# Kernel tuning notes

Hardware: AMD Instinct MI355X
Metric: run time of the kernel (lower is better)

## Reference

```python
import jax, jax.numpy as jnp
import numpy as np

GROUPS = 32
EPS = 1e-5
N_HEADS = 4


def group_norm(x, w, b):
    # x: [B, C, T]; GroupNorm over (C/G, T) within each of G groups
    B, C, T = x.shape
    xg = x.reshape(B, GROUPS, (C // GROUPS) * T)
    mean = xg.mean(axis=-1, keepdims=True)
    var = xg.var(axis=-1, keepdims=True)
    xn = ((xg - mean) * jax.lax.rsqrt(var + EPS)).reshape(B, C, T)
    return xn * w[None, :, None] + b[None, :, None]


def setup_inputs() -> dict:
    key = jax.random.key(0)
    ks = jax.random.split(key, 5)
    B, C, H, W = 2, 256, 64, 64
    x = jax.random.normal(ks[0], (B, C, H, W), dtype=jnp.float32)
    norm_w = jnp.ones((C,), dtype=jnp.float32)
    norm_b = jnp.zeros((C,), dtype=jnp.float32)
    qkv_w = jax.random.normal(ks[1], (3 * C, C), dtype=jnp.float32) * (C ** -0.5)
    qkv_b = jax.random.normal(ks[2], (3 * C,), dtype=jnp.float32) * 0.02
    proj_w = jax.random.normal(ks[3], (C, C), dtype=jnp.float32) * (C ** -0.5)
    proj_b = jax.random.normal(ks[4], (C,), dtype=jnp.float32) * 0.02
    return {"x": x, "norm_w": norm_w, "norm_b": norm_b,
            "qkv_w": qkv_w, "qkv_b": qkv_b,
            "proj_w": proj_w, "proj_b": proj_b}


def reference(x, norm_w, norm_b, qkv_w, qkv_b, proj_w, proj_b):
    B, C, Hs, Ws = x.shape
    T = Hs * Ws
    xf = x.reshape(B, C, T)
    xn = group_norm(xf, norm_w, norm_b)
    # 1x1 conv1d == channel matmul: [3C,C] x [B,C,T] -> [B,3C,T]
    qkv = jnp.einsum('oc,bct->bot', qkv_w, xn) + qkv_b[None, :, None]
    ch = C // N_HEADS
    # legacy order: [B, H*3*ch, T] -> [B*H, 3*ch, T] -> split
    qkv_h = qkv.reshape(B * N_HEADS, 3 * ch, T)
    q, k, v = qkv_h[:, :ch], qkv_h[:, ch:2 * ch], qkv_h[:, 2 * ch:]
    scale = ch ** -0.25
    # full [B*H, T, T] score matrix, softmax in fp32 (faithful to source)
    weight = jnp.einsum('bct,bcs->bts', q * scale, k * scale)
    weight = jax.nn.softmax(weight.astype(jnp.float32), axis=-1).astype(qkv.dtype)
    a = jnp.einsum('bts,bcs->bct', weight, v).reshape(B, C, T)
    h = jnp.einsum('oc,bct->bot', proj_w, a) + proj_b[None, :, None]
    return (xf + h).reshape(B, C, Hs, Ws)
```

## Files before the change

kernel.cpp:

```cpp
#include <hip/hip_runtime.h>
#include <hip/hip_bf16.h>

#define B_    2
#define C_    256
#define T_    4096
#define GRP   32
#define CPG   8
#define NH    4
#define CH    64
#define K3C   768
#define SPLIT 4
#define GSL   8
#define NSTAT (B_ * GRP * GSL)
#define NCVT  128
#define LOG2E 1.4426950408889634f

typedef __attribute__((ext_vector_type(8))) short bf16x8;
typedef __attribute__((ext_vector_type(4))) float f32x4;

#if __has_builtin(__builtin_amdgcn_exp2f)
#define EXP2(x) __builtin_amdgcn_exp2f(x)
#else
#define EXP2(x) exp2f(x)
#endif

__device__ __forceinline__ unsigned pk2(float a, float b) {
    __hip_bfloat162 h = __float22bfloat162_rn(make_float2(a, b));
    union { __hip_bfloat162 h2; unsigned u; } cv; cv.h2 = h;
    return cv.u;
}
__device__ __forceinline__ float bf2f(unsigned short u) {
    return __uint_as_float((unsigned)u << 16);
}

__device__ __forceinline__ void gl_lds16(const unsigned short* g, unsigned short* l) {
    __builtin_amdgcn_global_load_lds(
        (const __attribute__((address_space(1))) unsigned int*)g,
        (__attribute__((address_space(3))) unsigned int*)l,
        16, 0, 0);
}

__global__ __launch_bounds__(256) void pre_kernel(
    const float* __restrict__ x, float* __restrict__ stat,
    const float* __restrict__ qw, const float* __restrict__ pw,
    unsigned short* __restrict__ qwb, unsigned short* __restrict__ pwb) {
    int bid = blockIdx.x;
    int tid = threadIdx.x;
    if (bid < NSTAT) {
        int bg = bid >> 3, sl = bid & 7;
        const int SLN = CPG * T_ / GSL;
        const float* xp = x + (size_t)bg * CPG * T_ + (size_t)sl * SLN;
        float s = 0.f, s2 = 0.f;
        for (int i = tid * 4; i < SLN; i += 1024) {
            float4 v = *(const float4*)&xp[i];
            s  += (v.x + v.y) + (v.z + v.w);
            s2 += (v.x * v.x + v.y * v.y) + (v.z * v.z + v.w * v.w);
        }
        for (int off = 32; off > 0; off >>= 1) {
            s  += __shfl_down(s,  off);
            s2 += __shfl_down(s2, off);
        }
        __shared__ float rs[4], rs2[4];
        int wid = tid >> 6;
        if ((tid & 63) == 0) { rs[wid] = s; rs2[wid] = s2; }
        __syncthreads();
        if (tid == 0) {
            stat[bid * 2]     = (rs[0] + rs[1]) + (rs[2] + rs[3]);
            stat[bid * 2 + 1] = (rs2[0] + rs2[1]) + (rs2[2] + rs2[3]);
        }
    } else {
        int i = (bid - NSTAT) * 256 + tid;
        const int n1 = K3C * C_ / 8;
        const float* src; unsigned short* dst;
        if (i < n1) { src = qw + 8 * i; dst = qwb + 8 * i; }
        else { int j = i - n1; src = pw + 8 * j; dst = pwb + 8 * j; }
        float4 a = *(const float4*)src;
        float4 b = *(const float4*)(src + 4);
        uint4 u;
        u.x = pk2(a.x, a.y); u.y = pk2(a.z, a.w);
        u.z = pk2(b.x, b.y); u.w = pk2(b.z, b.w);
        *(uint4*)dst = u;
    }
}

__global__ __launch_bounds__(256) void gn_apply_kernel(
    const float* __restrict__ x, const float* __restrict__ stat,
    const float* __restrict__ w, const float* __restrict__ b,
    unsigned short* __restrict__ xnT) {
    int bg = blockIdx.x, sl = blockIdx.y;
    int batch = bg / GRP, g = bg % GRP;
    const float* xp = x + (size_t)bg * CPG * T_;
    int tid = threadIdx.x;

    float s = 0.f, s2 = 0.f;
#pragma unroll
    for (int i = 0; i < GSL; ++i) {
        s  += stat[(bg * GSL + i) * 2];
        s2 += stat[(bg * GSL + i) * 2 + 1];
    }
    float inv_n = 1.f / (float)(CPG * T_);
    float mean = s * inv_n;
    float var  = s2 * inv_n - mean * mean;
    float inv  = rsqrtf(var + 1e-5f);

    float wv[8], bv[8];
#pragma unroll
    for (int j = 0; j < 8; j++) {
        float ww = w[g * CPG + j] * inv;
        wv[j] = ww;
        bv[j] = b[g * CPG + j] - mean * ww;
    }
    unsigned short* op = xnT + (size_t)batch * T_ * C_ + g * CPG;
    int t0 = sl * (T_ / GSL);
#pragma unroll
    for (int rep = 0; rep < 2; ++rep) {
        int t = t0 + rep * 256 + tid;
        float v[8];
#pragma unroll
        for (int j = 0; j < 8; j++) v[j] = xp[(size_t)j * T_ + t] * wv[j] + bv[j];
        uint4 u;
        u.x = pk2(v[0], v[1]); u.y = pk2(v[2], v[3]);
        u.z = pk2(v[4], v[5]); u.w = pk2(v[6], v[7]);
        *(uint4*)&op[(size_t)t * C_] = u;
    }
}

__global__ __launch_bounds__(256) void qkv_gemm_kernel(
    const unsigned short* __restrict__ Wb, const float* __restrict__ bias,
    const unsigned short* __restrict__ Xt, unsigned short* __restrict__ q_t,
    unsigned short* __restrict__ k_t, unsigned short* __restrict__ v_d) {
    int tb = blockIdx.x * 128;
    int by = blockIdx.y;
    int bz = blockIdx.z;
    int ob = by * 64;
    int tid = threadIdx.x;
    int l = tid & 15, oct = (tid >> 4) & 3, w = tid >> 6;

    __shared__ __align__(16) unsigned short SH[64 * 264];

#pragma unroll
    for (int j = 0; j < 8; ++j) {
        int idx = tid + 256 * j;
        int row = idx >> 5, ch = idx & 31;
        *(uint4*)&SH[row * 264 + ch * 8] =
            *(const uint4*)&Wb[(size_t)(ob + row) * C_ + ch * 8];
    }
    __syncthreads();

    const unsigned short* Xb = Xt + (size_t)bz * T_ * C_;

    f32x4 acc[4][2];
#pragma unroll
    for (int mf = 0; mf < 4; ++mf)
#pragma unroll
        for (int nf = 0; nf < 2; ++nf) acc[mf][nf] = (f32x4){0.f, 0.f, 0.f, 0.f};

#pragma unroll
    for (int kk = 0; kk < 8; ++kk) {
        int c0 = 32 * kk + 8 * oct;
        bf16x8 bfr[2];
#pragma unroll
        for (int nf = 0; nf < 2; ++nf)
            bfr[nf] = *(const bf16x8*)&Xb[(size_t)(tb + 32 * w + 16 * nf + l) * C_ + c0];
#pragma unroll
        for (int mf = 0; mf < 4; ++mf) {
            bf16x8 af = *(const bf16x8*)&SH[(16 * mf + l) * 264 + c0];
#pragma unroll
            for (int nf = 0; nf < 2; ++nf)
                acc[mf][nf] = __builtin_amdgcn_mfma_f32_16x16x32_bf16(af, bfr[nf], acc[mf][nf], 0, 0, 0);
        }
    }

    int head = by / 3, sec = by - 3 * head;
    int bh = bz * NH + head;

    if (sec < 2) {
        float scale = (sec == 0) ? 0.125f * LOG2E : 1.f;
        unsigned short* dst = ((sec == 0) ? q_t : k_t) + (size_t)bh * T_ * CH;
#pragma unroll
        for (int mf = 0; mf < 4; ++mf) {
            float bvs[4];
#pragma unroll
            for (int r = 0; r < 4; ++r) bvs[r] = bias[ob + 16 * mf + 4 * oct + r];
#pragma unroll
            for (int nf = 0; nf < 2; ++nf) {
                int t = tb + 32 * w + 16 * nf + l;
                float v0 = (acc[mf][nf][0] + bvs[0]) * scale;
                float v1 = (acc[mf][nf][1] + bvs[1]) * scale;
                float v2 = (acc[mf][nf][2] + bvs[2]) * scale;
                float v3 = (acc[mf][nf][3] + bvs[3]) * scale;
                uint2 u; u.x = pk2(v0, v1); u.y = pk2(v2, v3);
                *(uint2*)&dst[(size_t)t * CH + 16 * mf + 4 * oct] = u;
            }
        }
    } else {
        __syncthreads();
#pragma unroll
        for (int mf = 0; mf < 4; ++mf) {
            float bvs[4];
#pragma unroll
            for (int r = 0; r < 4; ++r) bvs[r] = bias[ob + 16 * mf + 4 * oct + r];
#pragma unroll
            for (int nf = 0; nf < 2; ++nf) {
                int tl = 32 * w + 16 * nf + l;
#pragma unroll
                for (int r = 0; r < 4; ++r) {
                    unsigned pv = pk2(acc[mf][nf][r] + bvs[r], 0.f);
                    SH[(16 * mf + 4 * oct + r) * 136 + tl] = (unsigned short)(pv & 0xffffu);
                }
            }
        }
        __syncthreads();
        unsigned short* vdst = v_d + (size_t)bh * CH * T_;
#pragma unroll
        for (int j = 0; j < 4; ++j) {
            int idx = tid + 256 * j;
            int row = idx >> 4, ch = idx & 15;
            *(uint4*)&vdst[(size_t)row * T_ + tb + ch * 8] =
                *(uint4*)&SH[row * 136 + ch * 8];
        }
    }
}

__global__ __launch_bounds__(256, 3) void attn_kernel(
    const unsigned short* __restrict__ q_t, const unsigned short* __restrict__ k_t,
    const unsigned short* __restrict__ v_d, unsigned short* __restrict__ Opart,
    float* __restrict__ lbuf) {
    int bh = blockIdx.y;
    int sp = blockIdx.z;
    int t0 = blockIdx.x * 128;
    int tid = threadIdx.x;
    int l = tid & 15, q = (tid >> 4) & 3, w = tid >> 6;
    int lsw = l & 7;

    __shared__ __align__(16) unsigned short Kt[2][64 * 64];
    __shared__ __align__(16) unsigned short Vt[2][64 * 64];
    __shared__ __align__(16) unsigned short Ps[128 * 64];

    const unsigned short* qb = q_t + (size_t)bh * T_ * CH;
    const unsigned short* kb = k_t + (size_t)bh * T_ * CH;
    const unsigned short* vb = v_d + (size_t)bh * CH * T_;

    bf16x8 qf[2][2];
#pragma unroll
    for (int nf = 0; nf < 2; ++nf) {
        int t = t0 + 32 * w + 16 * nf + l;
#pragma unroll
        for (int kk = 0; kk < 2; ++kk)
            qf[nf][kk] = *(const bf16x8*)&qb[(size_t)t * CH + 32 * kk + 8 * q];
    }

    int ln = tid & 63;
    int rsub = ln >> 3;
    int cm8 = ((ln & 7) ^ rsub) * 8;
    int kr0 = 16 * w + rsub;

#define STAGE(buf, s0) do {                                                    \
    gl_lds16(kb + (size_t)((s0) + kr0) * CH + cm8,     &Kt[buf][(16 * w) * 64]);     \
    gl_lds16(kb + (size_t)((s0) + kr0 + 8) * CH + cm8, &Kt[buf][(16 * w + 8) * 64]); \
    gl_lds16(vb + (size_t)kr0 * T_ + (s0) + cm8,       &Vt[buf][(16 * w) * 64]);     \
    gl_lds16(vb + (size_t)(kr0 + 8) * T_ + (s0) + cm8, &Vt[buf][(16 * w + 8) * 64]); \
} while (0)

    f32x4 O[4][2];
#pragma unroll
    for (int mf = 0; mf < 4; ++mf)
#pragma unroll
        for (int nf = 0; nf < 2; ++nf) O[mf][nf] = (f32x4){0.f, 0.f, 0.f, 0.f};
    float l_run[2] = {0.f, 0.f};

    int s_beg = sp * (T_ / SPLIT);
    const int NT = (T_ / SPLIT) / 64;

    STAGE(0, s_beg);
    __syncthreads();

    int cur = 0;
    for (int t = 0; t < NT; ++t) {
        int s0n = s_beg + (t + 1) * 64;
        if (t + 1 < NT) STAGE(cur ^ 1, s0n);

        f32x4 S[4][2];
        __builtin_amdgcn_s_setprio(1);
#pragma unroll
        for (int sf = 0; sf < 4; ++sf) {
            f32x4 a0 = (f32x4){0.f, 0.f, 0.f, 0.f};
            f32x4 a1 = (f32x4){0.f, 0.f, 0.f, 0.f};
#pragma unroll
            for (int kk = 0; kk < 2; ++kk) {
                bf16x8 ka = *(const bf16x8*)
                    &Kt[cur][(16 * sf + l) * 64 + (((4 * kk + q) ^ lsw) * 8)];
                a0 = __builtin_amdgcn_mfma_f32_16x16x32_bf16(ka, qf[0][kk], a0, 0, 0, 0);
                a1 = __builtin_amdgcn_mfma_f32_16x16x32_bf16(ka, qf[1][kk], a1, 0, 0, 0);
            }
            S[sf][0] = a0; S[sf][1] = a1;
        }
        __builtin_amdgcn_s_setprio(0);

#pragma unroll
        for (int nf = 0; nf < 2; ++nf) {
            int trow = 32 * w + 16 * nf + l;
            float lloc = 0.f;
#pragma unroll
            for (int sf = 0; sf < 4; ++sf) {
                float p0 = EXP2(S[sf][nf][0]);
                float p1 = EXP2(S[sf][nf][1]);
                float p2 = EXP2(S[sf][nf][2]);
                float p3 = EXP2(S[sf][nf][3]);
                lloc += (p0 + p1) + (p2 + p3);
                uint2 u; u.x = pk2(p0, p1); u.y = pk2(p2, p3);
                *(uint2*)&Ps[trow * 64 + (((2 * sf + (q >> 1)) ^ lsw) * 8)
                             + (q & 1) * 4] = u;
            }
            l_run[nf] += lloc;
        }

#pragma unroll
        for (int kk = 0; kk < 2; ++kk) {
            bf16x8 pb[2];
#pragma unroll
            for (int nf = 0; nf < 2; ++nf)
                pb[nf] = *(const bf16x8*)
                    &Ps[(32 * w + 16 * nf + l) * 64 + (((4 * kk + q) ^ lsw) * 8)];
            __builtin_amdgcn_s_setprio(1);
#pragma unroll
            for (int mf = 0; mf < 4; ++mf) {
                bf16x8 va = *(const bf16x8*)
                    &Vt[cur][(16 * mf + l) * 64 + (((4 * kk + q) ^ lsw) * 8)];
#pragma unroll
                for (int nf = 0; nf < 2; ++nf)
                    O[mf][nf] = __builtin_amdgcn_mfma_f32_16x16x32_bf16(va, pb[nf], O[mf][nf], 0, 0, 0);
            }
            __builtin_amdgcn_s_setprio(0);
        }
        __syncthreads();
        cur ^= 1;
    }
#undef STAGE

#pragma unroll
    for (int nf = 0; nf < 2; ++nf) {
        float lt = l_run[nf];
        lt += __shfl_xor(lt, 16);
        lt += __shfl_xor(lt, 32);
        float inv = 1.f / lt;
        int t = t0 + 32 * w + 16 * nf + l;
        size_t row = (size_t)(sp * 8 + bh) * T_ + t;
        unsigned short* op = Opart + row * CH;
#pragma unroll
        for (int mf = 0; mf < 4; ++mf) {
            uint2 u;
            u.x = pk2(O[mf][nf][0] * inv, O[mf][nf][1] * inv);
            u.y = pk2(O[mf][nf][2] * inv, O[mf][nf][3] * inv);
            *(uint2*)&op[16 * mf + 4 * q] = u;
        }
        if (q == 0) lbuf[row] = lt;
    }
}

__global__ __launch_bounds__(256) void combine_kernel(
    const unsigned short* __restrict__ Opart, const float* __restrict__ lbuf,
    unsigned short* __restrict__ a_t) {
    int bx = blockIdx.x;
    int bh = bx >> 6;
    int tblk = bx & 63;
    int tid = threadIdx.x;
    int t = tblk * 64 + (tid >> 2);
    int sub = tid & 3;

    float lw[SPLIT];
    size_t rows[SPLIT];
    float lsum = 0.f;
#pragma unroll
    for (int sp = 0; sp < SPLIT; ++sp) {
        rows[sp] = (size_t)(sp * 8 + bh) * T_ + t;
        lw[sp] = lbuf[rows[sp]];
        lsum += lw[sp];
    }
    float inv = 1.f / lsum;

    float o[16];
#pragma unroll
    for (int i = 0; i < 16; ++i) o[i] = 0.f;
#pragma unroll
    for (int sp = 0; sp < SPLIT; ++sp) {
        float s = lw[sp] * inv;
        const unsigned short* p = Opart + rows[sp] * CH + sub * 16;
        uint4 u0 = *(const uint4*)p;
        uint4 u1 = *(const uint4*)(p + 8);
        unsigned us[8] = {u0.x, u0.y, u0.z, u0.w, u1.x, u1.y, u1.z, u1.w};
#pragma unroll
        for (int j = 0; j < 8; ++j) {
            o[2 * j]     += bf2f((unsigned short)(us[j] & 0xffffu)) * s;
            o[2 * j + 1] += bf2f((unsigned short)(us[j] >> 16)) * s;
        }
    }

    int batch = bh >> 2, h = bh & 3;
    unsigned short* dst = a_t + ((size_t)batch * T_ + t) * C_ + h * CH + sub * 16;
    uint4 u0, u1;
    u0.x = pk2(o[0], o[1]);   u0.y = pk2(o[2], o[3]);
    u0.z = pk2(o[4], o[5]);   u0.w = pk2(o[6], o[7]);
    u1.x = pk2(o[8], o[9]);   u1.y = pk2(o[10], o[11]);
    u1.z = pk2(o[12], o[13]); u1.w = pk2(o[14], o[15]);
    *(uint4*)dst = u0;
    *(uint4*)(dst + 8) = u1;
}

__global__ __launch_bounds__(256) void proj_gemm_kernel(
    const unsigned short* __restrict__ Wb, const float* __restrict__ bias,
    const unsigned short* __restrict__ At, const float* __restrict__ xres,
    float* __restrict__ out) {
    int tb = blockIdx.x * 64;
    int ob = blockIdx.y * 64;
    int bz = blockIdx.z;
    int tid = threadIdx.x;
    int l = tid & 15, oct = (tid >> 4) & 3, w = tid >> 6;

    __shared__ __align__(16) unsigned short SH[64 * 264];

#pragma unroll
    for (int j = 0; j < 8; ++j) {
        int idx = tid + 256 * j;
        int row = idx >> 5, ch = idx & 31;
        *(uint4*)&SH[row * 264 + ch * 8] =
            *(const uint4*)&Wb[(size_t)(ob + row) * C_ + ch * 8];
    }
    __syncthreads();

    const unsigned short* Ab = At + (size_t)bz * T_ * C_;
    int t = tb + 16 * w + l;

    f32x4 acc[4];
#pragma unroll
    for (int mf = 0; mf < 4; ++mf) acc[mf] = (f32x4){0.f, 0.f, 0.f, 0.f};

#pragma unroll
    for (int kk = 0; kk < 8; ++kk) {
        int c0 = 32 * kk + 8 * oct;
        bf16x8 bfr = *(const bf16x8*)&Ab[(size_t)t * C_ + c0];
#pragma unroll
        for (int mf = 0; mf < 4; ++mf) {
            bf16x8 af = *(const bf16x8*)&SH[(16 * mf + l) * 264 + c0];
            acc[mf] = __builtin_amdgcn_mfma_f32_16x16x32_bf16(af, bfr, acc[mf], 0, 0, 0);
        }
    }

#pragma unroll
    for (int mf = 0; mf < 4; ++mf) {
#pragma unroll
        for (int r = 0; r < 4; ++r) {
            int o = ob + 16 * mf + 4 * oct + r;
            size_t idx = ((size_t)bz * C_ + o) * T_ + t;
            out[idx] = acc[mf][r] + bias[o] + xres[idx];
        }
    }
}

extern "C" void kernel_launch(void* const* d_in, const int* in_sizes, int n_in,
                              void* d_out, int out_size, void* d_ws, size_t ws_size,
                              hipStream_t stream) {
    const float* x      = (const float*)d_in[0];
    const float* norm_w = (const float*)d_in[1];
    const float* norm_b = (const float*)d_in[2];
    const float* qkv_w  = (const float*)d_in[3];
    const float* qkv_b  = (const float*)d_in[4];
    const float* proj_w = (const float*)d_in[5];
    const float* proj_b = (const float*)d_in[6];
    float* out = (float*)d_out;

    char* p = (char*)d_ws;
    unsigned short* xnT = (unsigned short*)p; p += (size_t)B_ * T_ * C_ * 2;
    unsigned short* qwb = (unsigned short*)p; p += (size_t)K3C * C_ * 2;
    unsigned short* pwb = (unsigned short*)p; p += (size_t)C_ * C_ * 2;
    unsigned short* q_t = (unsigned short*)p; p += (size_t)B_ * NH * T_ * CH * 2;
    unsigned short* k_t = (unsigned short*)p; p += (size_t)B_ * NH * T_ * CH * 2;
    unsigned short* v_d = (unsigned short*)p; p += (size_t)B_ * NH * T_ * CH * 2;
    unsigned short* Opart = (unsigned short*)p; p += (size_t)SPLIT * 8 * T_ * CH * 2;
    float* lbuf         = (float*)p;          p += (size_t)SPLIT * 8 * T_ * 4;
    unsigned short* a_t = (unsigned short*)p; p += (size_t)B_ * T_ * C_ * 2;
    float* stat         = (float*)p;          p += (size_t)NSTAT * 2 * 4;

    pre_kernel<<<dim3(NSTAT + NCVT), dim3(256), 0, stream>>>(
        x, stat, qkv_w, proj_w, qwb, pwb);
    gn_apply_kernel<<<dim3(B_ * GRP, GSL), dim3(256), 0, stream>>>(
        x, stat, norm_w, norm_b, xnT);
    qkv_gemm_kernel<<<dim3(T_ / 128, 12, B_), dim3(256), 0, stream>>>(
        qwb, qkv_b, xnT, q_t, k_t, v_d);
    attn_kernel<<<dim3(T_ / 128, B_ * NH, SPLIT), dim3(256), 0, stream>>>(
        q_t, k_t, v_d, Opart, lbuf);
    combine_kernel<<<dim3(B_ * NH * (T_ / 64)), dim3(256), 0, stream>>>(Opart, lbuf, a_t);
    proj_gemm_kernel<<<dim3(T_ / 64, C_ / 64, B_), dim3(256), 0, stream>>>(
        pwb, proj_b, a_t, x, out);
}
```

Baseline: 149.7 us.

## Switch attention to 32x32x16 MFMA and pass P through registers via permlane32 swap

The attention kernel now uses 32x32x16 bf16 MFMA tiles instead of 16x16x32, so each wave handles a 32-query slab with two 32-key S accumulators. The exponentiated probabilities are repacked in registers with v_permlane32_swap instead of a round trip through the shared Ps buffer. This removes the Ps LDS writes and reads and frees shared memory, and the launch-bounds occupancy hint goes from 3 to 4 blocks. The larger accumulators (f32x16 per tile) raise register pressure, which may conflict with the higher occupancy target.

After: 146.9 us. About the same (-1.9%).

```diff
diff --git a/kernel.cpp b/kernel.cpp
--- a/kernel.cpp
+++ b/kernel.cpp
@@ -17,6 +17,7 @@
 
 typedef __attribute__((ext_vector_type(8))) short bf16x8;
 typedef __attribute__((ext_vector_type(4))) float f32x4;
+typedef __attribute__((ext_vector_type(16))) float f32x16;
 
 #if __has_builtin(__builtin_amdgcn_exp2f)
 #define EXP2(x) __builtin_amdgcn_exp2f(x)
@@ -222,7 +223,7 @@
     }
 }
 
-__global__ __launch_bounds__(256, 3) void attn_kernel(
+__global__ __launch_bounds__(256, 4) void attn_kernel(
     const unsigned short* __restrict__ q_t, const unsigned short* __restrict__ k_t,
     const unsigned short* __restrict__ v_d, unsigned short* __restrict__ Opart,
     float* __restrict__ lbuf) {
@@ -230,44 +231,41 @@
     int sp = blockIdx.z;
     int t0 = blockIdx.x * 128;
     int tid = threadIdx.x;
-    int l = tid & 15, q = (tid >> 4) & 3, w = tid >> 6;
-    int lsw = l & 7;
+    int ln = tid & 63;
+    int li = ln & 31;
+    int hi = ln >> 5;
+    int w  = tid >> 6;
+    int l7 = li & 7;
 
     __shared__ __align__(16) unsigned short Kt[2][64 * 64];
     __shared__ __align__(16) unsigned short Vt[2][64 * 64];
-    __shared__ __align__(16) unsigned short Ps[128 * 64];
 
     const unsigned short* qb = q_t + (size_t)bh * T_ * CH;
     const unsigned short* kb = k_t + (size_t)bh * T_ * CH;
     const unsigned short* vb = v_d + (size_t)bh * CH * T_;
 
-    bf16x8 qf[2][2];
-#pragma unroll
-    for (int nf = 0; nf < 2; ++nf) {
-        int t = t0 + 32 * w + 16 * nf + l;
-#pragma unroll
-        for (int kk = 0; kk < 2; ++kk)
-            qf[nf][kk] = *(const bf16x8*)&qb[(size_t)t * CH + 32 * kk + 8 * q];
-    }
-
-    int ln = tid & 63;
+    int tq = t0 + 32 * w + li;
+    bf16x8 qf[4];
+#pragma unroll
+    for (int ks = 0; ks < 4; ++ks)
+        qf[ks] = *(const bf16x8*)&qb[(size_t)tq * CH + ks * 16 + 8 * hi];
+
     int rsub = ln >> 3;
-    int cm8 = ((ln & 7) ^ rsub) * 8;
+    int sch  = ln & 7;
+    int cm8 = (sch ^ rsub) * 8;
     int kr0 = 16 * w + rsub;
 
-#define STAGE(buf, s0) do {                                                    \
+#define STAGE(buf, s0) do {                                                          \
     gl_lds16(kb + (size_t)((s0) + kr0) * CH + cm8,     &Kt[buf][(16 * w) * 64]);     \
     gl_lds16(kb + (size_t)((s0) + kr0 + 8) * CH + cm8, &Kt[buf][(16 * w + 8) * 64]); \
     gl_lds16(vb + (size_t)kr0 * T_ + (s0) + cm8,       &Vt[buf][(16 * w) * 64]);     \
     gl_lds16(vb + (size_t)(kr0 + 8) * T_ + (s0) + cm8, &Vt[buf][(16 * w + 8) * 64]); \
 } while (0)
 
-    f32x4 O[4][2];
-#pragma unroll
-    for (int mf = 0; mf < 4; ++mf)
-#pragma unroll
-        for (int nf = 0; nf < 2; ++nf) O[mf][nf] = (f32x4){0.f, 0.f, 0.f, 0.f};
-    float l_run[2] = {0.f, 0.f};
+    f32x16 O0, O1;
+#pragma unroll
+    for (int i = 0; i < 16; ++i) { O0[i] = 0.f; O1[i] = 0.f; }
+    float l_run = 0.f;
 
     int s_beg = sp * (T_ / SPLIT);
     const int NT = (T_ / SPLIT) / 64;
@@ -277,85 +275,91 @@
 
     int cur = 0;
     for (int t = 0; t < NT; ++t) {
-        int s0n = s_beg + (t + 1) * 64;
-        if (t + 1 < NT) STAGE(cur ^ 1, s0n);
-
-        f32x4 S[4][2];
+        if (t + 1 < NT) STAGE(cur ^ 1, s_beg + (t + 1) * 64);
+
+        f32x16 S0, S1;
+#pragma unroll
+        for (int i = 0; i < 16; ++i) { S0[i] = 0.f; S1[i] = 0.f; }
         __builtin_amdgcn_s_setprio(1);
 #pragma unroll
-        for (int sf = 0; sf < 4; ++sf) {
-            f32x4 a0 = (f32x4){0.f, 0.f, 0.f, 0.f};
-            f32x4 a1 = (f32x4){0.f, 0.f, 0.f, 0.f};
-#pragma unroll
-            for (int kk = 0; kk < 2; ++kk) {
-                bf16x8 ka = *(const bf16x8*)
-                    &Kt[cur][(16 * sf + l) * 64 + (((4 * kk + q) ^ lsw) * 8)];
-                a0 = __builtin_amdgcn_mfma_f32_16x16x32_bf16(ka, qf[0][kk], a0, 0, 0, 0);
-                a1 = __builtin_amdgcn_mfma_f32_16x16x32_bf16(ka, qf[1][kk], a1, 0, 0, 0);
+        for (int ks = 0; ks < 4; ++ks) {
+            bf16x8 ka0 = *(const bf16x8*)
+                &Kt[cur][li * 64 + (((2 * ks + hi) ^ l7) * 8)];
+            bf16x8 ka1 = *(const bf16x8*)
+                &Kt[cur][(32 + li) * 64 + (((2 * ks + hi) ^ l7) * 8)];
+            S0 = __builtin_amdgcn_mfma_f32_32x32x16_bf16(ka0, qf[ks], S0, 0, 0, 0);
+            S1 = __builtin_amdgcn_mfma_f32_32x32x16_bf16(ka1, qf[ks], S1, 0, 0, 0);
+        }
+        __builtin_amdgcn_s_setprio(0);
+
+        unsigned W0[8], W1[8];
+        float lloc = 0.f;
+#pragma unroll
+        for (int h = 0; h < 4; ++h) {
+            float a0 = EXP2(S0[4 * h + 0]), a1 = EXP2(S0[4 * h + 1]);
+            float a2 = EXP2(S0[4 * h + 2]), a3 = EXP2(S0[4 * h + 3]);
+            float b0 = EXP2(S1[4 * h + 0]), b1 = EXP2(S1[4 * h + 1]);
+            float b2 = EXP2(S1[4 * h + 2]), b3 = EXP2(S1[4 * h + 3]);
+            lloc += ((a0 + a1) + (a2 + a3)) + ((b0 + b1) + (b2 + b3));
+            W0[2 * h] = pk2(a0, a1); W0[2 * h + 1] = pk2(a2, a3);
+            W1[2 * h] = pk2(b0, b1); W1[2 * h + 1] = pk2(b2, b3);
+        }
+        l_run += lloc;
+
+        __builtin_amdgcn_s_setprio(1);
+#pragma unroll
+        for (int g = 0; g < 4; ++g) {
+            int ks = g & 1;
+            unsigned w0, w1, w2, w3;
+            if (g < 2) {
+                w0 = W0[4 * ks + 0]; w1 = W0[4 * ks + 1];
+                w2 = W0[4 * ks + 2]; w3 = W0[4 * ks + 3];
+            } else {
+                w0 = W1[4 * ks + 0]; w1 = W1[4 * ks + 1];
+                w2 = W1[4 * ks + 2]; w3 = W1[4 * ks + 3];
             }
-            S[sf][0] = a0; S[sf][1] = a1;
+            asm("v_permlane32_swap_b32 %0, %1" : "+v"(w0), "+v"(w2));
+            asm("v_permlane32_swap_b32 %0, %1" : "+v"(w1), "+v"(w3));
+            union { unsigned u[4]; bf16x8 v; } pu;
+            pu.u[0] = w0; pu.u[1] = w1; pu.u[2] = w2; pu.u[3] = w3;
+            bf16x8 va0 = *(const bf16x8*)
+                &Vt[cur][li * 64 + (((2 * g + hi) ^ l7) * 8)];
+            bf16x8 va1 = *(const bf16x8*)
+                &Vt[cur][(32 + li) * 64 + (((2 * g + hi) ^ l7) * 8)];
+            O0 = __builtin_amdgcn_mfma_f32_32x32x16_bf16(va0, pu.v, O0, 0, 0, 0);
+            O1 = __builtin_amdgcn_mfma_f32_32x32x16_bf16(va1, pu.v, O1, 0, 0, 0);
         }
         __builtin_amdgcn_s_setprio(0);
 
-#pragma unroll
-        for (int nf = 0; nf < 2; ++nf) {
-            int trow = 32 * w + 16 * nf + l;
-            float lloc = 0.f;
-#pragma unroll
-            for (int sf = 0; sf < 4; ++sf) {
-                float p0 = EXP2(S[sf][nf][0]);
-                float p1 = EXP2(S[sf][nf][1]);
-                float p2 = EXP2(S[sf][nf][2]);
-                float p3 = EXP2(S[sf][nf][3]);
-                lloc += (p0 + p1) + (p2 + p3);
-                uint2 u; u.x = pk2(p0, p1); u.y = pk2(p2, p3);
-                *(uint2*)&Ps[trow * 64 + (((2 * sf + (q >> 1)) ^ lsw) * 8)
-                             + (q & 1) * 4] = u;
-            }
-            l_run[nf] += lloc;
-        }
-
-#pragma unroll
-        for (int kk = 0; kk < 2; ++kk) {
-            bf16x8 pb[2];
-#pragma unroll
-            for (int nf = 0; nf < 2; ++nf)
-                pb[nf] = *(const bf16x8*)
-                    &Ps[(32 * w + 16 * nf + l) * 64 + (((4 * kk + q) ^ lsw) * 8)];
-            __builtin_amdgcn_s_setprio(1);
-#pragma unroll
-            for (int mf = 0; mf < 4; ++mf) {
-                bf16x8 va = *(const bf16x8*)
-                    &Vt[cur][(16 * mf + l) * 64 + (((4 * kk + q) ^ lsw) * 8)];
-#pragma unroll
-                for (int nf = 0; nf < 2; ++nf)
-                    O[mf][nf] = __builtin_amdgcn_mfma_f32_16x16x32_bf16(va, pb[nf], O[mf][nf], 0, 0, 0);
-            }
-            __builtin_amdgcn_s_setprio(0);
-        }
         __syncthreads();
         cur ^= 1;
     }
 #undef STAGE
 
-#pragma unroll
-    for (int nf = 0; nf < 2; ++nf) {
-        float lt = l_run[nf];
-        lt += __shfl_xor(lt, 16);
-        lt += __shfl_xor(lt, 32);
-        float inv = 1.f / lt;
-        int t = t0 + 32 * w + 16 * nf + l;
-        size_t row = (size_t)(sp * 8 + bh) * T_ + t;
-        unsigned short* op = Opart + row * CH;
-#pragma unroll
-        for (int mf = 0; mf < 4; ++mf) {
+    float lt = l_run + __shfl_xor(l_run, 32);
+    float inv = 1.f / lt;
+    size_t row = (size_t)(sp * 8 + bh) * T_ + tq;
+    unsigned short* op = Opart + row * CH;
+#pragma unroll
+    for (int cb = 0; cb < 2; ++cb) {
+#pragma unroll
+        for (int h = 0; h < 4; ++h) {
+            int c = 32 * cb + 8 * h + 4 * hi;
+            float v0, v1, v2, v3;
+            if (cb == 0) {
+                v0 = O0[4 * h + 0]; v1 = O0[4 * h + 1];
+                v2 = O0[4 * h + 2]; v3 = O0[4 * h + 3];
+            } else {
+                v0 = O1[4 * h + 0]; v1 = O1[4 * h + 1];
+                v2 = O1[4 * h + 2]; v3 = O1[4 * h + 3];
+            }
             uint2 u;
-            u.x = pk2(O[mf][nf][0] * inv, O[mf][nf][1] * inv);
-            u.y = pk2(O[mf][nf][2] * inv, O[mf][nf][3] * inv);
-            *(uint2*)&op[16 * mf + 4 * q] = u;
-        }
-        if (q == 0) lbuf[row] = lt;
-    }
+            u.x = pk2(v0 * inv, v1 * inv);
+            u.y = pk2(v2 * inv, v3 * inv);
+            *(uint2*)&op[c] = u;
+        }
+    }
+    if (hi == 0) lbuf[row] = lt;
 }
 
 __global__ __launch_bounds__(256) void combine_kernel(
```
